# Kernel optimization log

Measured on AMD Instinct MI355X. Metric: run time of the kernel, lower is better.

Reference implementation:

```python
import jax, jax.numpy as jnp
import numpy as np
import math

B = 524288
D = 4
CTX = 64
HID = 128
IN_DIM = 2 + CTX  # keep_idx len is 2 for every mask
# default_masks_D(4, 10) dedups to exactly these 4 masks (torch module therefore has 4 layers)
KEEP = ((0, 1), (1, 2), (2, 3), (0, 3))
TRANS = ((2, 3), (0, 3), (0, 1), (1, 2))
L = 4


def _mlp(x, W1, b1, W2, b2, W3, b3):
    # MLP(in_dim, out_dim, hidden=128, depth=2): Lin+GELU, Lin+GELU, Lin
    x = jax.nn.gelu(x @ W1 + b1, approximate=False)
    x = jax.nn.gelu(x @ W2 + b2, approximate=False)
    return x @ W3 + b3


def setup_inputs() -> dict:
    key = jax.random.key(0)
    ks = jax.random.split(key, 16)
    theta = jax.random.normal(ks[0], (B, D), dtype=jnp.float32)
    h = jax.random.normal(ks[1], (B, CTX), dtype=jnp.float32)
    p = lambda k, shape: jax.random.normal(k, shape, dtype=jnp.float32) * 0.02
    inp = {"theta": theta, "h": h}
    # stacked per-layer weights for s_net and t_net
    for pref, off in (("s", 2), ("t", 8)):
        inp[pref + "W1"] = p(ks[off + 0], (L, IN_DIM, HID))
        inp[pref + "b1"] = p(ks[off + 1], (L, HID))
        inp[pref + "W2"] = p(ks[off + 2], (L, HID, HID))
        inp[pref + "b2"] = p(ks[off + 3], (L, HID))
        inp[pref + "W3"] = p(ks[off + 4], (L, HID, 2))
        inp[pref + "b3"] = p(ks[off + 5], (L, 2))
    return inp


def reference(theta, h, sW1, sb1, sW2, sb2, sW3, sb3, tW1, tb1, tW2, tb2, tW3, tb3):
    # ConditionalRealNVP.log_prob(theta, h)
    x = theta
    logdet = jnp.zeros(theta.shape[0], dtype=theta.dtype)
    for i in range(L):
        keep = np.array(KEEP[i])
        trans = np.array(TRANS[i])
        xp = jnp.concatenate([x[:, keep], h], axis=1)  # [B, 66]
        s = _mlp(xp, sW1[i], sb1[i], sW2[i], sb2[i], sW3[i], sb3[i])  # [B, 2]
        t = _mlp(xp, tW1[i], tb1[i], tW2[i], tb2[i], tW3[i], tb3[i])  # [B, 2]
        x = x.at[:, trans].set(x[:, trans] * jnp.exp(s) + t)
        logdet = logdet + s.sum(axis=1)
    log_pz = -0.5 * (x ** 2).sum(axis=1) - 0.5 * D * math.log(2 * math.pi)
    return log_pz + logdet
```

## Files before the change

### kernel.cpp

```cpp
#include <hip/hip_runtime.h>
#include <hip/hip_bf16.h>

typedef short short8 __attribute__((ext_vector_type(8)));
typedef float f32x4 __attribute__((ext_vector_type(4)));
typedef float f32x2 __attribute__((ext_vector_type(2)));
typedef unsigned short u16;
typedef unsigned int u32;
typedef u32 u32x4 __attribute__((ext_vector_type(4)));

#define NL_STRIDE 57344
#define OFF_W1F 0
#define OFF_W2F 16384
#define OFF_W3F 49152
#define OFF_W1K 53248
#define OFF_B1  54272
#define OFF_B2  54784
#define OFF_B3  55296

__device__ __forceinline__ u16 f2bf(float f) {
  union { float f; unsigned int u; } v; v.f = f;
  unsigned int r = v.u + 0x7fffu + ((v.u >> 16) & 1u);
  return (u16)(r >> 16);
}

__device__ __forceinline__ u32 cvt_pk_bf16(float lo, float hi) {
  u32 r;
  asm("v_cvt_pk_bf16_f32 %0, %1, %2" : "=v"(r) : "v"(lo), "v"(hi));
  return r;
}

__device__ __forceinline__ f32x2 gelu2(f32x2 x) {
  f32x2 u = x * x;
  f32x2 t = u * 0.00417617f + (-0.0560330f);
  t = t * u + 0.394326f;
  f32x2 s = x * t + 0.5f;
  s.x = __builtin_amdgcn_fmed3f(s.x, 0.0f, 1.0f);
  s.y = __builtin_amdgcn_fmed3f(s.y, 0.0f, 1.0f);
  return x * s;
}

__device__ __forceinline__ int perm_col(int p) {
  return (p & ~31) | ((p & 1) << 4) | ((p & 31) >> 1);
}

__global__ __launch_bounds__(256) void prep_kernel(
    const float* __restrict__ sW1, const float* __restrict__ sb1,
    const float* __restrict__ sW2, const float* __restrict__ sb2,
    const float* __restrict__ sW3, const float* __restrict__ sb3,
    const float* __restrict__ tW1, const float* __restrict__ tb1,
    const float* __restrict__ tW2, const float* __restrict__ tb2,
    const float* __restrict__ tW3, const float* __restrict__ tb3,
    char* __restrict__ ws)
{
  int nl = blockIdx.x;
  int layer = nl >> 1, net = nl & 1;
  const float* W1 = net ? tW1 : sW1;
  const float* W2 = net ? tW2 : sW2;
  const float* W3 = net ? tW3 : sW3;
  const float* B1 = net ? tb1 : sb1;
  const float* B2 = net ? tb2 : sb2;
  const float* B3 = net ? tb3 : sb3;
  char* base = ws + (size_t)nl * NL_STRIDE;
  int e = blockIdx.y * 256 + (int)threadIdx.x;

  if (e < 8192) {
    int kt = e >> 12, rem = e & 4095, nt = rem >> 9, r2 = rem & 511;
    int l = r2 >> 3, j = r2 & 7;
    int k = kt * 32 + (l >> 4) * 8 + j, n = nt * 16 + (l & 15);
    ((u16*)(base + OFF_W1F))[e] = f2bf(W1[layer * 8448 + (2 + k) * 128 + n]);
  } else if (e < 24576) {
    int e2 = e - 8192;
    int kt = e2 >> 12, nt = (e2 >> 9) & 7, l = (e2 >> 3) & 63, j = e2 & 7;
    int kp = kt * 32 + (l >> 4) * 8 + j, n = nt * 16 + (l & 15);
    int c = perm_col(kp);
    ((u16*)(base + OFF_W2F))[e2] = f2bf(W2[layer * 16384 + c * 128 + n]);
  } else if (e < 26624) {
    int e3 = e - 24576;
    int kt = e3 >> 9, l = (e3 >> 3) & 63, j = e3 & 7;
    int kp = kt * 32 + (l >> 4) * 8 + j, n = l & 15;
    int c = perm_col(kp);
    float v = (n < 2) ? W3[layer * 256 + c * 2 + n] : 0.0f;
    ((u16*)(base + OFF_W3F))[e3] = f2bf(v);
  } else if (e < 26880) {
    int e4 = e - 26624; int r = e4 >> 7, n = e4 & 127;
    ((float*)(base + OFF_W1K))[e4] = W1[layer * 8448 + r * 128 + n];
  } else if (e < 27008) {
    int e5 = e - 26880; ((float*)(base + OFF_B1))[e5] = B1[layer * 128 + e5];
  } else if (e < 27136) {
    int e6 = e - 27008; ((float*)(base + OFF_B2))[e6] = B2[layer * 128 + e6];
  } else if (e < 27138) {
    int e7 = e - 27136; ((float*)(base + OFF_B3))[e7] = B3[layer * 2 + e7];
  }
}

__global__ __launch_bounds__(256, 3) void realnvp_kernel(
    const float* __restrict__ theta, const float* __restrict__ h_g,
    const char* __restrict__ ws, float* __restrict__ out)
{
  __shared__ __align__(16) u16 hs[128 * 64];
  __shared__ __align__(16) u16 hid[128 * 128];
  __shared__ __align__(16) float x_lds[128 * 4];
  __shared__ __align__(8)  float xk_lds[128 * 2];
  __shared__ float sbuf[2 * 128 * 2];

  const int tid = (int)threadIdx.x;
  const int row0 = (int)blockIdx.x * 128;
  const int wv = tid >> 6, lane = tid & 63, q = lane >> 4, lr = lane & 15;
  const char* hsB = (const char*)hs;
  char* hidB = (char*)hid;
  const int swz = (lr & 7) << 4;

  if (tid < 128) {
    float4 t4 = *(const float4*)(theta + (size_t)(row0 + tid) * 4);
    *(f32x4*)&x_lds[tid * 4] = (f32x4){t4.x, t4.y, t4.z, t4.w};
    xk_lds[tid * 2 + 0] = t4.x;
    xk_lds[tid * 2 + 1] = t4.y;
  }
  {
    int r = tid >> 1, hf = tid & 1;
    const float* src = h_g + (size_t)(row0 + r) * 64 + hf * 32;
    const int wswz = (r & 7) << 4;
#pragma unroll
    for (int c = 0; c < 32; c += 8) {
      float4 f0 = *(const float4*)(src + c);
      float4 f1 = *(const float4*)(src + c + 4);
      u32x4 o;
      o[0] = cvt_pk_bf16(f0.x, f0.y);
      o[1] = cvt_pk_bf16(f0.z, f0.w);
      o[2] = cvt_pk_bf16(f1.x, f1.y);
      o[3] = cvt_pk_bf16(f1.z, f1.w);
      *(u32x4*)((char*)hs + (((r * 64 + hf * 32 + c) * 2) ^ wswz)) = o;
    }
  }
  __syncthreads();

  float logdet = 0.0f;
  const f32x4 zero4 = {0.f, 0.f, 0.f, 0.f};
  const int col0 = wv * 32 + lr;

  unsigned wb[4];
#pragma unroll
  for (int r = 0; r < 4; ++r) {
    int rl = q * 4 + r;
    wb[r] = (unsigned)((rl * 256 + wv * 64 + lr * 4) ^ ((rl & 7) << 4));
  }

#pragma unroll 1
  for (int layer = 0; layer < 4; ++layer) {
#pragma unroll 1
    for (int net = 0; net < 2; ++net) {
      const char* base = ws + (size_t)(layer * 2 + net) * NL_STRIDE;
      const u16* w1f = (const u16*)(base + OFF_W1F);
      const u16* w2f = (const u16*)(base + OFF_W2F);
      const u16* w3f = (const u16*)(base + OFF_W3F);
      const float* w1k = (const float*)(base + OFF_W1K);
      const float* b1 = (const float*)(base + OFF_B1);
      const float* b2 = (const float*)(base + OFF_B2);
      const float* b3 = (const float*)(base + OFF_B3);

      f32x4 acc[8][2];
#pragma unroll
      for (int mt = 0; mt < 8; ++mt) { acc[mt][0] = zero4; acc[mt][1] = zero4; }
#pragma unroll
      for (int kt = 0; kt < 2; ++kt) {
        const int abase = (((lr * 64 + kt * 32 + q * 8) * 2)) ^ swz;
        short8 a[8];
#pragma unroll
        for (int mt = 0; mt < 8; ++mt)
          a[mt] = *(const short8*)(hsB + abase + mt * 2048);
        short8 b0 = *(const short8*)(w1f + (kt * 8 + wv * 2 + 0) * 512 + lane * 8);
        short8 b1v = *(const short8*)(w1f + (kt * 8 + wv * 2 + 1) * 512 + lane * 8);
#pragma unroll
        for (int mt = 0; mt < 8; ++mt) {
          acc[mt][0] = __builtin_amdgcn_mfma_f32_16x16x32_bf16(a[mt], b0, acc[mt][0], 0, 0, 0);
          acc[mt][1] = __builtin_amdgcn_mfma_f32_16x16x32_bf16(a[mt], b1v, acc[mt][1], 0, 0, 0);
        }
      }
      f32x2 wk0 = {w1k[col0],       w1k[col0 + 16]};
      f32x2 wk1 = {w1k[128 + col0], w1k[128 + col0 + 16]};
      f32x2 bb  = {b1[col0],        b1[col0 + 16]};
      __syncthreads();
#pragma unroll
      for (int mt = 0; mt < 8; ++mt) {
#pragma unroll
        for (int r = 0; r < 4; ++r) {
          int row = mt * 16 + q * 4 + r;
          f32x2 xk = *(const f32x2*)(xk_lds + row * 2);
          f32x2 v = (f32x2){acc[mt][0][r], acc[mt][1][r]} + bb;
          v = xk.x * wk0 + v;
          v = xk.y * wk1 + v;
          f32x2 g = gelu2(v);
          *(u32*)(hidB + (wb[r] + mt * 4096)) = cvt_pk_bf16(g.x, g.y);
        }
      }
      __syncthreads();

      f32x4 acc2[8][2];
#pragma unroll
      for (int mt = 0; mt < 8; ++mt) { acc2[mt][0] = zero4; acc2[mt][1] = zero4; }
#pragma unroll
      for (int kt = 0; kt < 4; ++kt) {
        const int abase = ((lr * 256 + kt * 64 + q * 16)) ^ swz;
        short8 a[8];
#pragma unroll
        for (int mt = 0; mt < 8; ++mt)
          a[mt] = *(const short8*)(hidB + abase + mt * 4096);
        short8 b0 = *(const short8*)(w2f + (kt * 8 + wv * 2 + 0) * 512 + lane * 8);
        short8 b1v = *(const short8*)(w2f + (kt * 8 + wv * 2 + 1) * 512 + lane * 8);
#pragma unroll
        for (int mt = 0; mt < 8; ++mt) {
          acc2[mt][0] = __builtin_amdgcn_mfma_f32_16x16x32_bf16(a[mt], b0, acc2[mt][0], 0, 0, 0);
          acc2[mt][1] = __builtin_amdgcn_mfma_f32_16x16x32_bf16(a[mt], b1v, acc2[mt][1], 0, 0, 0);
        }
      }
      f32x2 cbb = {b2[col0], b2[col0 + 16]};
      __syncthreads();
#pragma unroll
      for (int mt = 0; mt < 8; ++mt) {
#pragma unroll
        for (int r = 0; r < 4; ++r) {
          f32x2 v = (f32x2){acc2[mt][0][r], acc2[mt][1][r]} + cbb;
          f32x2 g = gelu2(v);
          *(u32*)(hidB + (wb[r] + mt * 4096)) = cvt_pk_bf16(g.x, g.y);
        }
      }
      __syncthreads();

      f32x4 acc3[2]; acc3[0] = zero4; acc3[1] = zero4;
#pragma unroll
      for (int kt = 0; kt < 4; ++kt) {
        short8 b = *(const short8*)(w3f + kt * 512 + lane * 8);
        const int abase = ((lr * 256 + kt * 64 + q * 16)) ^ swz;
#pragma unroll
        for (int i = 0; i < 2; ++i) {
          short8 a = *(const short8*)(hidB + abase + (wv * 2 + i) * 4096);
          acc3[i] = __builtin_amdgcn_mfma_f32_16x16x32_bf16(a, b, acc3[i], 0, 0, 0);
        }
      }
      if (lr < 2) {
        float bbv = b3[lr];
#pragma unroll
        for (int i = 0; i < 2; ++i) {
          int rb = (wv * 2 + i) * 16 + q * 4;
#pragma unroll
          for (int r = 0; r < 4; ++r)
            sbuf[net * 256 + (rb + r) * 2 + lr] = acc3[i][r] + bbv;
        }
      }
      __syncthreads();
    }

    if (tid < 128) {
      float s0 = sbuf[tid * 2 + 0], s1 = sbuf[tid * 2 + 1];
      float t0 = sbuf[256 + tid * 2 + 0], t1 = sbuf[256 + tid * 2 + 1];
      int a0 = (0x1002 >> (layer * 4)) & 15;
      int a1 = (0x2133 >> (layer * 4)) & 15;
      x_lds[tid * 4 + a0] = x_lds[tid * 4 + a0] * __expf(s0) + t0;
      x_lds[tid * 4 + a1] = x_lds[tid * 4 + a1] * __expf(s1) + t1;
      logdet += s0 + s1;
      int nl_ = (layer + 1) & 3;
      int nk0 = (0x0210 >> (nl_ * 4)) & 15;
      int nk1 = (0x3321 >> (nl_ * 4)) & 15;
      xk_lds[tid * 2 + 0] = x_lds[tid * 4 + nk0];
      xk_lds[tid * 2 + 1] = x_lds[tid * 4 + nk1];
    }
    __syncthreads();
  }

  if (tid < 128) {
    float x0 = x_lds[tid * 4 + 0], x1 = x_lds[tid * 4 + 1];
    float x2 = x_lds[tid * 4 + 2], x3 = x_lds[tid * 4 + 3];
    out[row0 + tid] = -0.5f * (x0 * x0 + x1 * x1 + x2 * x2 + x3 * x3)
                      - 3.6757541328f + logdet;
  }
}

extern "C" void kernel_launch(void* const* d_in, const int* in_sizes, int n_in,
                              void* d_out, int out_size, void* d_ws, size_t ws_size,
                              hipStream_t stream) {
  (void)in_sizes; (void)n_in; (void)out_size; (void)ws_size;
  const float* theta = (const float*)d_in[0];
  const float* h     = (const float*)d_in[1];
  const float* sW1 = (const float*)d_in[2],  *sb1 = (const float*)d_in[3];
  const float* sW2 = (const float*)d_in[4],  *sb2 = (const float*)d_in[5];
  const float* sW3 = (const float*)d_in[6],  *sb3 = (const float*)d_in[7];
  const float* tW1 = (const float*)d_in[8],  *tb1 = (const float*)d_in[9];
  const float* tW2 = (const float*)d_in[10], *tb2 = (const float*)d_in[11];
  const float* tW3 = (const float*)d_in[12], *tb3 = (const float*)d_in[13];
  float* out = (float*)d_out;
  char* ws = (char*)d_ws;

  dim3 pgrid(8, 107);
  prep_kernel<<<pgrid, 256, 0, stream>>>(sW1, sb1, sW2, sb2, sW3, sb3,
                                         tW1, tb1, tW2, tb2, tW3, tb3, ws);
  realnvp_kernel<<<4096, 256, 0, stream>>>(theta, h, (const char*)ws, out);
}
```

Measured before the change: 582.2 us.

## Halve rows per block to 64, raise occupancy, add MFMA priority hints

Each block now handles 64 rows instead of 128, which halves the LDS footprint and accumulator registers. The launch bound goes from 3 to 5 blocks per SM and the grid doubles. The epilogue is restructured: xk is stored transposed in LDS, and the per-column GELU is vectorised across row pairs. s_setprio hints are placed around the MFMA loops. In exchange, weight loads from global/L2 double per row processed and there are more barriers per row.

```diff
diff --git a/kernel.cpp b/kernel.cpp
--- a/kernel.cpp
+++ b/kernel.cpp
@@ -28,6 +28,8 @@
   asm("v_cvt_pk_bf16_f32 %0, %1, %2" : "=v"(r) : "v"(lo), "v"(hi));
   return r;
 }
+
+__device__ __forceinline__ f32x2 bc2(float s) { return (f32x2){s, s}; }
 
 __device__ __forceinline__ f32x2 gelu2(f32x2 x) {
   f32x2 u = x * x;
@@ -93,35 +95,35 @@
   }
 }
 
-__global__ __launch_bounds__(256, 3) void realnvp_kernel(
+__global__ __launch_bounds__(256, 5) void realnvp_kernel(
     const float* __restrict__ theta, const float* __restrict__ h_g,
     const char* __restrict__ ws, float* __restrict__ out)
 {
-  __shared__ __align__(16) u16 hs[128 * 64];
-  __shared__ __align__(16) u16 hid[128 * 128];
-  __shared__ __align__(16) float x_lds[128 * 4];
-  __shared__ __align__(8)  float xk_lds[128 * 2];
-  __shared__ float sbuf[2 * 128 * 2];
+  __shared__ __align__(16) u16 hs[64 * 64];
+  __shared__ __align__(16) u16 hid[64 * 128];
+  __shared__ __align__(16) float x_lds[64 * 4];
+  __shared__ __align__(8)  float xk_lds[2 * 64];
+  __shared__ float sbuf[2 * 64 * 2];
 
   const int tid = (int)threadIdx.x;
-  const int row0 = (int)blockIdx.x * 128;
+  const int row0 = (int)blockIdx.x * 64;
   const int wv = tid >> 6, lane = tid & 63, q = lane >> 4, lr = lane & 15;
   const char* hsB = (const char*)hs;
   char* hidB = (char*)hid;
   const int swz = (lr & 7) << 4;
 
-  if (tid < 128) {
+  if (tid < 64) {
     float4 t4 = *(const float4*)(theta + (size_t)(row0 + tid) * 4);
     *(f32x4*)&x_lds[tid * 4] = (f32x4){t4.x, t4.y, t4.z, t4.w};
-    xk_lds[tid * 2 + 0] = t4.x;
-    xk_lds[tid * 2 + 1] = t4.y;
+    xk_lds[tid]      = t4.x;
+    xk_lds[64 + tid] = t4.y;
   }
   {
-    int r = tid >> 1, hf = tid & 1;
-    const float* src = h_g + (size_t)(row0 + r) * 64 + hf * 32;
+    int r = tid >> 2, hf = tid & 3;
+    const float* src = h_g + (size_t)(row0 + r) * 64 + hf * 16;
     const int wswz = (r & 7) << 4;
 #pragma unroll
-    for (int c = 0; c < 32; c += 8) {
+    for (int c = 0; c < 16; c += 8) {
       float4 f0 = *(const float4*)(src + c);
       float4 f1 = *(const float4*)(src + c + 4);
       u32x4 o;
@@ -129,7 +131,7 @@
       o[1] = cvt_pk_bf16(f0.z, f0.w);
       o[2] = cvt_pk_bf16(f1.x, f1.y);
       o[3] = cvt_pk_bf16(f1.z, f1.w);
-      *(u32x4*)((char*)hs + (((r * 64 + hf * 32 + c) * 2) ^ wswz)) = o;
+      *(u32x4*)((char*)hs + (((r * 64 + hf * 16 + c) * 2) ^ wswz)) = o;
     }
   }
   __syncthreads();
@@ -158,101 +160,107 @@
       const float* b2 = (const float*)(base + OFF_B2);
       const float* b3 = (const float*)(base + OFF_B3);
 
-      f32x4 acc[8][2];
-#pragma unroll
-      for (int mt = 0; mt < 8; ++mt) { acc[mt][0] = zero4; acc[mt][1] = zero4; }
+      f32x4 acc[4][2];
+#pragma unroll
+      for (int mt = 0; mt < 4; ++mt) { acc[mt][0] = zero4; acc[mt][1] = zero4; }
+      __builtin_amdgcn_s_setprio(1);
 #pragma unroll
       for (int kt = 0; kt < 2; ++kt) {
         const int abase = (((lr * 64 + kt * 32 + q * 8) * 2)) ^ swz;
-        short8 a[8];
-#pragma unroll
-        for (int mt = 0; mt < 8; ++mt)
+        short8 a[4];
+#pragma unroll
+        for (int mt = 0; mt < 4; ++mt)
           a[mt] = *(const short8*)(hsB + abase + mt * 2048);
         short8 b0 = *(const short8*)(w1f + (kt * 8 + wv * 2 + 0) * 512 + lane * 8);
         short8 b1v = *(const short8*)(w1f + (kt * 8 + wv * 2 + 1) * 512 + lane * 8);
 #pragma unroll
-        for (int mt = 0; mt < 8; ++mt) {
+        for (int mt = 0; mt < 4; ++mt) {
           acc[mt][0] = __builtin_amdgcn_mfma_f32_16x16x32_bf16(a[mt], b0, acc[mt][0], 0, 0, 0);
           acc[mt][1] = __builtin_amdgcn_mfma_f32_16x16x32_bf16(a[mt], b1v, acc[mt][1], 0, 0, 0);
         }
       }
-      f32x2 wk0 = {w1k[col0],       w1k[col0 + 16]};
-      f32x2 wk1 = {w1k[128 + col0], w1k[128 + col0 + 16]};
-      f32x2 bb  = {b1[col0],        b1[col0 + 16]};
-      __syncthreads();
-#pragma unroll
-      for (int mt = 0; mt < 8; ++mt) {
-#pragma unroll
-        for (int r = 0; r < 4; ++r) {
-          int row = mt * 16 + q * 4 + r;
-          f32x2 xk = *(const f32x2*)(xk_lds + row * 2);
-          f32x2 v = (f32x2){acc[mt][0][r], acc[mt][1][r]} + bb;
-          v = xk.x * wk0 + v;
-          v = xk.y * wk1 + v;
-          f32x2 g = gelu2(v);
-          *(u32*)(hidB + (wb[r] + mt * 4096)) = cvt_pk_bf16(g.x, g.y);
+      __builtin_amdgcn_s_setprio(0);
+      float wk00 = w1k[col0],       wk01 = w1k[col0 + 16];
+      float wk10 = w1k[128 + col0], wk11 = w1k[128 + col0 + 16];
+      float bb0 = b1[col0], bb1 = b1[col0 + 16];
+      __syncthreads();
+#pragma unroll
+      for (int mt = 0; mt < 4; ++mt) {
+        int rb = mt * 16 + q * 4;
+#pragma unroll
+        for (int p = 0; p < 2; ++p) {
+          int row = rb + 2 * p;
+          f32x2 xk0 = *(const f32x2*)(xk_lds + row);
+          f32x2 xk1 = *(const f32x2*)(xk_lds + 64 + row);
+          f32x2 vA = {acc[mt][0][2 * p], acc[mt][0][2 * p + 1]};
+          f32x2 vB = {acc[mt][1][2 * p], acc[mt][1][2 * p + 1]};
+          vA = vA + bc2(bb0); vA = xk0 * bc2(wk00) + vA; vA = xk1 * bc2(wk10) + vA;
+          vB = vB + bc2(bb1); vB = xk0 * bc2(wk01) + vB; vB = xk1 * bc2(wk11) + vB;
+          f32x2 gA = gelu2(vA), gB = gelu2(vB);
+          *(u32*)(hidB + (wb[2 * p]     + mt * 4096)) = cvt_pk_bf16(gA.x, gB.x);
+          *(u32*)(hidB + (wb[2 * p + 1] + mt * 4096)) = cvt_pk_bf16(gA.y, gB.y);
         }
       }
       __syncthreads();
 
-      f32x4 acc2[8][2];
-#pragma unroll
-      for (int mt = 0; mt < 8; ++mt) { acc2[mt][0] = zero4; acc2[mt][1] = zero4; }
+      f32x4 acc2[4][2];
+#pragma unroll
+      for (int mt = 0; mt < 4; ++mt) { acc2[mt][0] = zero4; acc2[mt][1] = zero4; }
+      __builtin_amdgcn_s_setprio(1);
 #pragma unroll
       for (int kt = 0; kt < 4; ++kt) {
         const int abase = ((lr * 256 + kt * 64 + q * 16)) ^ swz;
-        short8 a[8];
-#pragma unroll
-        for (int mt = 0; mt < 8; ++mt)
+        short8 a[4];
+#pragma unroll
+        for (int mt = 0; mt < 4; ++mt)
           a[mt] = *(const short8*)(hidB + abase + mt * 4096);
         short8 b0 = *(const short8*)(w2f + (kt * 8 + wv * 2 + 0) * 512 + lane * 8);
         short8 b1v = *(const short8*)(w2f + (kt * 8 + wv * 2 + 1) * 512 + lane * 8);
 #pragma unroll
-        for (int mt = 0; mt < 8; ++mt) {
+        for (int mt = 0; mt < 4; ++mt) {
           acc2[mt][0] = __builtin_amdgcn_mfma_f32_16x16x32_bf16(a[mt], b0, acc2[mt][0], 0, 0, 0);
           acc2[mt][1] = __builtin_amdgcn_mfma_f32_16x16x32_bf16(a[mt], b1v, acc2[mt][1], 0, 0, 0);
         }
       }
-      f32x2 cbb = {b2[col0], b2[col0 + 16]};
-      __syncthreads();
-#pragma unroll
-      for (int mt = 0; mt < 8; ++mt) {
-#pragma unroll
-        for (int r = 0; r < 4; ++r) {
-          f32x2 v = (f32x2){acc2[mt][0][r], acc2[mt][1][r]} + cbb;
-          f32x2 g = gelu2(v);
-          *(u32*)(hidB + (wb[r] + mt * 4096)) = cvt_pk_bf16(g.x, g.y);
+      __builtin_amdgcn_s_setprio(0);
+      float cb0 = b2[col0], cb1 = b2[col0 + 16];
+      __syncthreads();
+#pragma unroll
+      for (int mt = 0; mt < 4; ++mt) {
+#pragma unroll
+        for (int p = 0; p < 2; ++p) {
+          f32x2 vA = {acc2[mt][0][2 * p], acc2[mt][0][2 * p + 1]};
+          f32x2 vB = {acc2[mt][1][2 * p], acc2[mt][1][2 * p + 1]};
+          vA = vA + bc2(cb0);
+          vB = vB + bc2(cb1);
+          f32x2 gA = gelu2(vA), gB = gelu2(vB);
+          *(u32*)(hidB + (wb[2 * p]     + mt * 4096)) = cvt_pk_bf16(gA.x, gB.x);
+          *(u32*)(hidB + (wb[2 * p + 1] + mt * 4096)) = cvt_pk_bf16(gA.y, gB.y);
         }
       }
       __syncthreads();
 
-      f32x4 acc3[2]; acc3[0] = zero4; acc3[1] = zero4;
+      f32x4 acc3 = zero4;
 #pragma unroll
       for (int kt = 0; kt < 4; ++kt) {
         short8 b = *(const short8*)(w3f + kt * 512 + lane * 8);
         const int abase = ((lr * 256 + kt * 64 + q * 16)) ^ swz;
-#pragma unroll
-        for (int i = 0; i < 2; ++i) {
-          short8 a = *(const short8*)(hidB + abase + (wv * 2 + i) * 4096);
-          acc3[i] = __builtin_amdgcn_mfma_f32_16x16x32_bf16(a, b, acc3[i], 0, 0, 0);
-        }
+        short8 a = *(const short8*)(hidB + abase + wv * 4096);
+        acc3 = __builtin_amdgcn_mfma_f32_16x16x32_bf16(a, b, acc3, 0, 0, 0);
       }
       if (lr < 2) {
         float bbv = b3[lr];
-#pragma unroll
-        for (int i = 0; i < 2; ++i) {
-          int rb = (wv * 2 + i) * 16 + q * 4;
-#pragma unroll
-          for (int r = 0; r < 4; ++r)
-            sbuf[net * 256 + (rb + r) * 2 + lr] = acc3[i][r] + bbv;
-        }
+        int rb = wv * 16 + q * 4;
+#pragma unroll
+        for (int r = 0; r < 4; ++r)
+          sbuf[net * 128 + (rb + r) * 2 + lr] = acc3[r] + bbv;
       }
       __syncthreads();
     }
 
-    if (tid < 128) {
+    if (tid < 64) {
       float s0 = sbuf[tid * 2 + 0], s1 = sbuf[tid * 2 + 1];
-      float t0 = sbuf[256 + tid * 2 + 0], t1 = sbuf[256 + tid * 2 + 1];
+      float t0 = sbuf[128 + tid * 2 + 0], t1 = sbuf[128 + tid * 2 + 1];
       int a0 = (0x1002 >> (layer * 4)) & 15;
       int a1 = (0x2133 >> (layer * 4)) & 15;
       x_lds[tid * 4 + a0] = x_lds[tid * 4 + a0] * __expf(s0) + t0;
@@ -261,13 +269,13 @@
       int nl_ = (layer + 1) & 3;
       int nk0 = (0x0210 >> (nl_ * 4)) & 15;
       int nk1 = (0x3321 >> (nl_ * 4)) & 15;
-      xk_lds[tid * 2 + 0] = x_lds[tid * 4 + nk0];
-      xk_lds[tid * 2 + 1] = x_lds[tid * 4 + nk1];
+      xk_lds[tid]      = x_lds[tid * 4 + nk0];
+      xk_lds[64 + tid] = x_lds[tid * 4 + nk1];
     }
     __syncthreads();
   }
 
-  if (tid < 128) {
+  if (tid < 64) {
     float x0 = x_lds[tid * 4 + 0], x1 = x_lds[tid * 4 + 1];
     float x2 = x_lds[tid * 4 + 2], x3 = x_lds[tid * 4 + 3];
     out[row0 + tid] = -0.5f * (x0 * x0 + x1 * x1 + x2 * x2 + x3 * x3)
@@ -293,5 +301,5 @@
   dim3 pgrid(8, 107);
   prep_kernel<<<pgrid, 256, 0, stream>>>(sW1, sb1, sW2, sb2, sW3, sb3,
                                          tW1, tb1, tW2, tb2, tW3, tb3, ws);
-  realnvp_kernel<<<4096, 256, 0, stream>>>(theta, h, (const char*)ws, out);
-}
+  realnvp_kernel<<<8192, 256, 0, stream>>>(theta, h, (const char*)ws, out);
+}
```

Result: faster. 526.7 us (-9.5%).
